# Kernel tuning notes

Measured on AMD Instinct MI355X. Metric: run time of the kernel, lower is better.

The kernel has to match this reference:

```python
import jax, jax.numpy as jnp
import numpy as np

SL, BS, E, H, PF, STRIDE, SHIFT = 2048, 2, 1024, 16, 16, 1, 0
DH = E // H  # 64


def setup_inputs() -> dict:
    key = jax.random.key(0)
    ks = jax.random.split(key, 6)
    s = 0.02
    return {
        'x': jax.random.normal(ks[0], (SL, BS, E), jnp.float32),
        'ln_g': jnp.ones((E,), jnp.float32),
        'ln_b': jnp.zeros((E,), jnp.float32),
        'Wq': jax.random.normal(ks[1], (E, E), jnp.float32) * s,
        'bq': jnp.zeros((E,), jnp.float32),
        'Wk': jax.random.normal(ks[2], (E, E), jnp.float32) * s,
        'bk': jnp.zeros((E,), jnp.float32),
        'Wv': jax.random.normal(ks[3], (E, E), jnp.float32) * s,
        'bv': jnp.zeros((E,), jnp.float32),
        'Wo': jax.random.normal(ks[4], (E, E), jnp.float32) * s,
        'bo': jnp.zeros((E,), jnp.float32),
    }


def _layernorm(x, g, b, eps=1e-5):
    m = x.mean(-1, keepdims=True)
    v = jnp.var(x, axis=-1, keepdims=True)
    return (x - m) * jax.lax.rsqrt(v + eps) * g + b


def _sparsify(context, h):
    # faithful to sparsify(): r = (arange(h)+1)*stride - pf + shift (+ arange(pf)), mod c
    c = context.shape[0]
    base = (jnp.arange(h) + 1) * STRIDE - PF + SHIFT          # [h]
    idx = (base[None, :] + jnp.arange(PF)[:, None]) % c       # [pf, h]
    return context[idx.reshape(-1)].reshape(PF, h, context.shape[1], context.shape[2])


def reference(x, ln_g, ln_b, Wq, bq, Wk, bk, Wv, bv, Wo, bo):
    sl, bs, e = x.shape
    residual = x
    xn = _layernorm(x, ln_g, ln_b)
    # gather pf-sized local context window per query position (modular wrap)
    fetch = _sparsify(xn, sl)                                  # [pf, sl, bs, E]
    # per-token query (length-1) attending to its pf gathered keys
    q = (xn @ Wq + bq).reshape(sl, bs, H, DH)                  # [sl,bs,H,dh]
    k = (fetch @ Wk + bk).reshape(PF, sl, bs, H, DH)           # [pf,sl,bs,H,dh]
    v = (fetch @ Wv + bv).reshape(PF, sl, bs, H, DH)
    scale = 1.0 / jnp.sqrt(jnp.float32(DH))
    scores = jnp.einsum('sbhd,psbhd->sbhp', q, k) * scale      # [sl,bs,H,pf]
    attn = jax.nn.softmax(scores, axis=-1)
    out = jnp.einsum('sbhp,psbhd->sbhd', attn, v).reshape(sl, bs, e)
    out = out @ Wo + bo                                        # output projection
    # dropout is a no-op in eval
    return residual + out
```

## Files before the change

kernel.cpp:

```cpp
#include <hip/hip_runtime.h>
#include <cstdint>
#include <cstddef>

#define SLEN 2048
#define BSZ  2
#define EDIM 1024
#define NHEAD 16
#define DHEAD 64
#define PFW  16
#define NTOK (SLEN*BSZ)

typedef __attribute__((ext_vector_type(8))) short short8;
typedef __attribute__((ext_vector_type(4))) float floatx4;
typedef __attribute__((ext_vector_type(4))) int   int4v;

__device__ __forceinline__ short f2bf(float f) {
  union { float f; uint32_t u; } v; v.f = f;
  uint32_t r = v.u + 0x7fffu + ((v.u >> 16) & 1u);
  return (short)(r >> 16);
}
__device__ __forceinline__ float bf2f(short s) {
  union { uint32_t u; float f; } v; v.u = ((uint32_t)(uint16_t)s) << 16;
  return v.f;
}
__device__ __forceinline__ int q8(float f, float inv) {
  int q = __float2int_rn(f * inv);
  return min(127, max(-127, q));
}

__device__ __forceinline__ void async16(const void* g, void* l) {
  __builtin_amdgcn_global_load_lds((const __attribute__((address_space(1))) void*)g,
                                   (__attribute__((address_space(3))) void*)l,
                                   16, 0, 0);
}

__global__ __launch_bounds__(256) void prep_kernel(
    const float* __restrict__ x, const float* __restrict__ g,
    const float* __restrict__ b, char* __restrict__ xn_i8,
    float* __restrict__ xn_scl,
    const float* __restrict__ W0, const float* __restrict__ W1,
    const float* __restrict__ W2, const float* __restrict__ W3,
    short* __restrict__ Wt_base)
{
  const int bid = blockIdx.x;
  const int tid = threadIdx.x;

  if (bid < NTOK) {
    const int row = bid;
    const float4 v = ((const float4*)(x + (size_t)row * EDIM))[tid];
    float s  = v.x + v.y + v.z + v.w;
    float ss = v.x * v.x + v.y * v.y + v.z * v.z + v.w * v.w;
#pragma unroll
    for (int off = 32; off; off >>= 1) {
      s  += __shfl_xor(s, off);
      ss += __shfl_xor(ss, off);
    }
    __shared__ float ws_s[4], ws_ss[4], ws_m[4];
    const int lane = tid & 63, wave = tid >> 6;
    if (lane == 0) { ws_s[wave] = s; ws_ss[wave] = ss; }
    __syncthreads();
    s  = ws_s[0] + ws_s[1] + ws_s[2] + ws_s[3];
    ss = ws_ss[0] + ws_ss[1] + ws_ss[2] + ws_ss[3];

    const float mean = s * (1.0f / EDIM);
    const float var  = ss * (1.0f / EDIM) - mean * mean;
    const float rs   = rsqrtf(var + 1e-5f);

    const float4 gv = ((const float4*)g)[tid];
    const float4 bv = ((const float4*)b)[tid];
    const float n0 = (v.x - mean) * rs * gv.x + bv.x;
    const float n1 = (v.y - mean) * rs * gv.y + bv.y;
    const float n2 = (v.z - mean) * rs * gv.z + bv.z;
    const float n3 = (v.w - mean) * rs * gv.w + bv.w;

    float am = fmaxf(fmaxf(fabsf(n0), fabsf(n1)), fmaxf(fabsf(n2), fabsf(n3)));
#pragma unroll
    for (int off = 32; off; off >>= 1) am = fmaxf(am, __shfl_xor(am, off));
    if (lane == 0) ws_m[wave] = am;
    __syncthreads();
    am = fmaxf(fmaxf(ws_m[0], ws_m[1]), fmaxf(ws_m[2], ws_m[3]));

    const float inv = (am > 1e-30f) ? 127.0f / am : 0.0f;
    const int q0 = q8(n0, inv), q1 = q8(n1, inv), q2 = q8(n2, inv), q3 = q8(n3, inv);
    const uint32_t pack = (uint32_t)(q0 & 0xff) | ((uint32_t)(q1 & 0xff) << 8) |
                          ((uint32_t)(q2 & 0xff) << 16) | ((uint32_t)(q3 & 0xff) << 24);
    ((uint32_t*)(xn_i8 + (size_t)row * EDIM))[tid] = pack;
    if (tid == 0) xn_scl[row] = am * (1.0f / 127.0f);
  } else {
    const int t = bid - NTOK;
    const int z = t >> 10;
    const int rem = t & 1023;
    const int n0 = (rem & 31) * 32;
    const int k0 = (rem >> 5) * 32;
    const float* W = (z == 0) ? W0 : (z == 1) ? W1 : (z == 2) ? W2 : W3;
    short* Wt = Wt_base + (size_t)z * EDIM * EDIM;

    __shared__ float tile[32][33];
    const int tx = tid & 31;
    const int ty = tid >> 5;
#pragma unroll
    for (int i = 0; i < 4; ++i)
      tile[ty + i * 8][tx] = W[(size_t)(k0 + ty + i * 8) * EDIM + n0 + tx];
    __syncthreads();
#pragma unroll
    for (int i = 0; i < 4; ++i)
      Wt[(size_t)(n0 + ty + i * 8) * EDIM + k0 + tx] = f2bf(tile[tx][ty + i * 8]);
  }
}

__global__ __launch_bounds__(256) void quant_w(
    const short* __restrict__ Wt, char* __restrict__ w_i8,
    float* __restrict__ w_scl)
{
  const int R = blockIdx.x;
  const int tid = threadIdx.x;
  const short4 s4 = ((const short4*)(Wt + (size_t)R * EDIM))[tid];
  const float w0 = bf2f(s4.x), w1 = bf2f(s4.y), w2 = bf2f(s4.z), w3 = bf2f(s4.w);

  float am = fmaxf(fmaxf(fabsf(w0), fabsf(w1)), fmaxf(fabsf(w2), fabsf(w3)));
#pragma unroll
  for (int off = 32; off; off >>= 1) am = fmaxf(am, __shfl_xor(am, off));
  __shared__ float wm[4];
  const int lane = tid & 63, wave = tid >> 6;
  if (lane == 0) wm[wave] = am;
  __syncthreads();
  am = fmaxf(fmaxf(wm[0], wm[1]), fmaxf(wm[2], wm[3]));

  const float inv = (am > 1e-30f) ? 127.0f / am : 0.0f;
  const int q0 = q8(w0, inv), q1 = q8(w1, inv), q2 = q8(w2, inv), q3 = q8(w3, inv);
  const uint32_t pack = (uint32_t)(q0 & 0xff) | ((uint32_t)(q1 & 0xff) << 8) |
                        ((uint32_t)(q2 & 0xff) << 16) | ((uint32_t)(q3 & 0xff) << 24);
  ((uint32_t*)(w_i8 + (size_t)R * EDIM))[tid] = pack;
  if (tid == 0) w_scl[R] = am * (1.0f / 127.0f);
}

__global__ __launch_bounds__(256) void gemm_qkv_i8(
    const char* __restrict__ xn_i8, const float* __restrict__ xn_scl,
    const char* __restrict__ w_i8, const float* __restrict__ w_scl,
    const float* __restrict__ bq, const float* __restrict__ bk,
    const float* __restrict__ bv, short* __restrict__ qkv_base)
{
  __shared__ __align__(16) char As[128 * 64];
  __shared__ __align__(16) char Bs[128 * 64];

  const int bid  = blockIdx.x;
  const int xcd  = bid & 7;
  const int slot = bid >> 3;
  const int nz   = xcd * 3 + slot / 32;
  const int mt   = slot & 31;
  const int z    = nz >> 3;
  const int nt   = nz & 7;

  const char*  Bt   = w_i8 + (size_t)z * EDIM * EDIM;
  const float* bscl = w_scl + z * EDIM;
  const float* bias = (z == 0) ? bq : (z == 1) ? bk : bv;
  short* out        = qkv_base + (size_t)z * NTOK * EDIM;

  const int bm = mt * 128;
  const int bn = nt * 128;
  const int tid  = threadIdx.x;
  const int lane = tid & 63;
  const int wave = tid >> 6;

  int4v acc[4][4];
#pragma unroll
  for (int i = 0; i < 4; ++i)
#pragma unroll
    for (int j = 0; j < 4; ++j) { int4v zz = {0, 0, 0, 0}; acc[i][j] = zz; }

  const int lrow  = lane >> 2;
  const int lcolB = (lane & 3) * 16;
  const char* gA0 = xn_i8 + (size_t)(bm + wave * 32 + lrow) * EDIM + lcolB;
  const char* gA1 = gA0 + (size_t)16 * EDIM;
  const char* gB0 = Bt + (size_t)(bn + wave * 32 + lrow) * EDIM + lcolB;
  const char* gB1 = gB0 + (size_t)16 * EDIM;
  char* lA0 = As + wave * 2048;
  char* lA1 = lA0 + 1024;
  char* lB0 = Bs + wave * 2048;
  char* lB1 = lB0 + 1024;

  const int wm  = (wave >> 1) * 64;
  const int wn  = (wave & 1) * 64;
  const int fr  = lane & 15;
  const int fqB = (lane >> 4) * 16;

  for (int k0 = 0; k0 < EDIM; k0 += 64) {
    async16(gA0, lA0); async16(gA1, lA1);
    async16(gB0, lB0); async16(gB1, lB1);
    gA0 += 64; gA1 += 64; gB0 += 64; gB1 += 64;
    __syncthreads();

    int4v af[4], bf[4];
#pragma unroll
    for (int mi = 0; mi < 4; ++mi)
      af[mi] = *(const int4v*)(As + (size_t)(wm + mi * 16 + fr) * 64 + fqB);
#pragma unroll
    for (int ni = 0; ni < 4; ++ni)
      bf[ni] = *(const int4v*)(Bs + (size_t)(wn + ni * 16 + fr) * 64 + fqB);
#pragma unroll
    for (int mi = 0; mi < 4; ++mi)
#pragma unroll
      for (int ni = 0; ni < 4; ++ni)
        acc[mi][ni] = __builtin_amdgcn_mfma_i32_16x16x64_i8(
            af[mi], bf[ni], acc[mi][ni], 0, 0, 0);
    __syncthreads();
  }

  const int r0 = bm + wm + ((lane >> 4) * 4);
  const int c0 = bn + wn + (lane & 15);
#pragma unroll
  for (int mi = 0; mi < 4; ++mi) {
    float sa[4];
#pragma unroll
    for (int r = 0; r < 4; ++r) sa[r] = xn_scl[r0 + mi * 16 + r];
#pragma unroll
    for (int ni = 0; ni < 4; ++ni) {
      const int4v v = acc[mi][ni];
      const int col = c0 + ni * 16;
      const float sb = bscl[col];
      const float bb = bias[col];
#pragma unroll
      for (int r = 0; r < 4; ++r) {
        const int row = r0 + mi * 16 + r;
        out[(size_t)row * EDIM + col] = f2bf((float)v[r] * (sa[r] * sb) + bb);
      }
    }
  }
}

__global__ __launch_bounds__(256) void gemm_o_i8(
    const char* __restrict__ A8, const float* __restrict__ a_scl,
    const char* __restrict__ w_i8, const float* __restrict__ w_scl,
    const float* __restrict__ bo, const float* __restrict__ residual,
    float* __restrict__ out)
{
  __shared__ __align__(16) char As[64 * 64];
  __shared__ __align__(16) char Bs[128 * 64];
  __shared__ float sa_lds[64 * 17];

  const int bm = blockIdx.x * 64;
  const int bn = blockIdx.y * 128;
  const int tid  = threadIdx.x;
  const int lane = tid & 63;
  const int wave = tid >> 6;

#pragma unroll
  for (int i = 0; i < 4; ++i) {
    const int e = tid + i * 256;
    const int row = e >> 4, h = e & 15;
    sa_lds[row * 17 + h] = a_scl[(size_t)(bm + row) * NHEAD + h];
  }

  floatx4 facc[2][4];
#pragma unroll
  for (int i = 0; i < 2; ++i)
#pragma unroll
    for (int j = 0; j < 4; ++j) { floatx4 zz = {0.f, 0.f, 0.f, 0.f}; facc[i][j] = zz; }

  const int lrow  = lane >> 2;
  const int lcolB = (lane & 3) * 16;
  const char* gA0 = A8 + (size_t)(bm + wave * 16 + lrow) * EDIM + lcolB;
  const char* gB0 = w_i8 + (size_t)3 * EDIM * EDIM +
                    (size_t)(bn + wave * 32 + lrow) * EDIM + lcolB;
  const char* gB1 = gB0 + (size_t)16 * EDIM;
  char* lA0 = As + wave * 1024;
  char* lB0 = Bs + wave * 2048;
  char* lB1 = lB0 + 1024;

  const int wm  = (wave >> 1) * 32;
  const int wn  = (wave & 1) * 64;
  const int fr  = lane & 15;
  const int fqB = (lane >> 4) * 16;
  const int q4  = lane >> 4;

  for (int ki = 0; ki < 16; ++ki) {
    async16(gA0, lA0);
    async16(gB0, lB0); async16(gB1, lB1);
    gA0 += 64; gB0 += 64; gB1 += 64;
    __syncthreads();

    int4v af[2], bf[4];
#pragma unroll
    for (int mi = 0; mi < 2; ++mi)
      af[mi] = *(const int4v*)(As + (size_t)(wm + mi * 16 + fr) * 64 + fqB);
#pragma unroll
    for (int ni = 0; ni < 4; ++ni)
      bf[ni] = *(const int4v*)(Bs + (size_t)(wn + ni * 16 + fr) * 64 + fqB);

    float sa_v[2][4];
#pragma unroll
    for (int mi = 0; mi < 2; ++mi)
#pragma unroll
      for (int r = 0; r < 4; ++r)
        sa_v[mi][r] = sa_lds[(wm + mi * 16 + q4 * 4 + r) * 17 + ki];

#pragma unroll
    for (int mi = 0; mi < 2; ++mi)
#pragma unroll
      for (int ni = 0; ni < 4; ++ni) {
        const int4v zz = {0, 0, 0, 0};
        const int4v t = __builtin_amdgcn_mfma_i32_16x16x64_i8(
            af[mi], bf[ni], zz, 0, 0, 0);
#pragma unroll
        for (int r = 0; r < 4; ++r)
          facc[mi][ni][r] += sa_v[mi][r] * (float)t[r];
      }
    __syncthreads();
  }

  const int r0 = bm + wm + q4 * 4;
  const int c0 = bn + wn + (lane & 15);
#pragma unroll
  for (int mi = 0; mi < 2; ++mi)
#pragma unroll
    for (int ni = 0; ni < 4; ++ni) {
      const int col = c0 + ni * 16;
      const float sb = w_scl[3 * EDIM + col];
      const float bb = bo[col];
#pragma unroll
      for (int r = 0; r < 4; ++r) {
        const int row = r0 + mi * 16 + r;
        const size_t idx = (size_t)row * EDIM + col;
        out[idx] = residual[idx] + facc[mi][ni][r] * sb + bb;
      }
    }
}

#define VT_LD 80
#define PB_LD 40

__global__ __launch_bounds__(256) void attn_mfma(
    const short* __restrict__ Q, const short* __restrict__ K,
    const short* __restrict__ V, char* __restrict__ O8,
    float* __restrict__ a_scl)
{
  const int tid  = threadIdx.x;
  const int lane = tid & 63;
  const int wave = tid >> 6;
  const int quad = lane >> 4;
  const int l16  = lane & 15;

  const int bh = blockIdx.y;
  const int h  = bh & (NHEAD - 1);
  const int b  = bh >> 4;
  const int s_blk = blockIdx.x * 64;
  const int col0  = h * DHEAD;

  __shared__ __align__(16) short VT[64 * VT_LD];
  __shared__ __align__(16) short Pb[4][16 * PB_LD];

  for (int task = tid; task < 320; task += 256) {
    const int kp  = task >> 3;
    const int dg  = task & 7;
    const int kk0 = kp * 2;
    int sA = s_blk - 15 + kk0;
    int sB = sA + 1;
    if (sA < 0) sA += SLEN;  if (sA >= SLEN) sA -= SLEN;
    if (sB < 0) sB += SLEN;  if (sB >= SLEN) sB -= SLEN;
    const short8 vA = *(const short8*)(V + (size_t)(sA * BSZ + b) * EDIM + col0 + dg * 8);
    const short8 vB = *(const short8*)(V + (size_t)(sB * BSZ + b) * EDIM + col0 + dg * 8);
#pragma unroll
    for (int j = 0; j < 8; ++j) {
      const int d = dg * 8 + j;
      const uint32_t pack = (uint32_t)(uint16_t)vA[j] | ((uint32_t)(uint16_t)vB[j] << 16);
      *(uint32_t*)&VT[d * VT_LD + kk0] = pack;
    }
  }

  const int sw = s_blk + wave * 16;
  short8 aq[2];
  {
    const size_t base = (size_t)((sw + l16) * BSZ + b) * EDIM + col0 + quad * 8;
    aq[0] = *(const short8*)(Q + base);
    aq[1] = *(const short8*)(Q + base + 32);
  }
  short8 bkf[2][2];
#pragma unroll
  for (int T = 0; T < 2; ++T) {
    int ks = sw - 15 + T * 16 + l16;
    if (ks < 0) ks += SLEN;
    if (ks >= SLEN) ks -= SLEN;
    const size_t base = (size_t)(ks * BSZ + b) * EDIM + col0 + quad * 8;
    bkf[T][0] = *(const short8*)(K + base);
    bkf[T][1] = *(const short8*)(K + base + 32);
  }

  floatx4 S[2];
  { floatx4 zz = {0.f, 0.f, 0.f, 0.f}; S[0] = zz; S[1] = zz; }
#pragma unroll
  for (int T = 0; T < 2; ++T) {
    S[T] = __builtin_amdgcn_mfma_f32_16x16x32_bf16(aq[0], bkf[T][0], S[T], 0, 0, 0);
    S[T] = __builtin_amdgcn_mfma_f32_16x16x32_bf16(aq[1], bkf[T][1], S[T], 0, 0, 0);
  }

  float sc[2][4];
#pragma unroll
  for (int T = 0; T < 2; ++T)
#pragma unroll
    for (int r = 0; r < 4; ++r) {
      const int m = quad * 4 + r;
      const int c = T * 16 + l16;
      const int d = c - m;
      sc[T][r] = (d >= 0 && d <= 15) ? S[T][r] * 0.125f : -1e30f;
    }
  float mx[4], sm[4];
#pragma unroll
  for (int r = 0; r < 4; ++r) mx[r] = fmaxf(sc[0][r], sc[1][r]);
#pragma unroll
  for (int off = 1; off <= 8; off <<= 1)
#pragma unroll
    for (int r = 0; r < 4; ++r) mx[r] = fmaxf(mx[r], __shfl_xor(mx[r], off));
  float p[2][4];
#pragma unroll
  for (int r = 0; r < 4; ++r) {
    p[0][r] = __expf(sc[0][r] - mx[r]);
    p[1][r] = __expf(sc[1][r] - mx[r]);
    sm[r] = p[0][r] + p[1][r];
  }
#pragma unroll
  for (int off = 1; off <= 8; off <<= 1)
#pragma unroll
    for (int r = 0; r < 4; ++r) sm[r] += __shfl_xor(sm[r], off);

  __syncthreads();

  short* Pw = Pb[wave];
#pragma unroll
  for (int T = 0; T < 2; ++T)
#pragma unroll
    for (int r = 0; r < 4; ++r) {
      const int m = quad * 4 + r;
      const int c = T * 16 + l16;
      Pw[m * PB_LD + c] = f2bf(p[T][r]);
    }
  __syncthreads();
  const short8 ap = *(const short8*)(Pw + l16 * PB_LD + quad * 8);

  floatx4 Oacc[4];
  { floatx4 zz = {0.f, 0.f, 0.f, 0.f}; Oacc[0] = zz; Oacc[1] = zz; Oacc[2] = zz; Oacc[3] = zz; }
#pragma unroll
  for (int nt = 0; nt < 4; ++nt) {
    const short8 bv = *(const short8*)(VT + (nt * 16 + l16) * VT_LD + wave * 16 + quad * 8);
    Oacc[nt] = __builtin_amdgcn_mfma_f32_16x16x32_bf16(ap, bv, Oacc[nt], 0, 0, 0);
  }

  float vv[4][4];
  float am[4] = {0.f, 0.f, 0.f, 0.f};
#pragma unroll
  for (int nt = 0; nt < 4; ++nt)
#pragma unroll
    for (int r = 0; r < 4; ++r) {
      const float v = Oacc[nt][r] / sm[r];
      vv[nt][r] = v;
      am[r] = fmaxf(am[r], fabsf(v));
    }
#pragma unroll
  for (int off = 1; off <= 8; off <<= 1)
#pragma unroll
    for (int r = 0; r < 4; ++r) am[r] = fmaxf(am[r], __shfl_xor(am[r], off));

  float inv[4];
#pragma unroll
  for (int r = 0; r < 4; ++r) inv[r] = (am[r] > 1e-30f) ? 127.0f / am[r] : 0.0f;

#pragma unroll
  for (int nt = 0; nt < 4; ++nt)
#pragma unroll
    for (int r = 0; r < 4; ++r) {
      const int m = quad * 4 + r;
      const int row = (sw + m) * BSZ + b;
      O8[(size_t)row * EDIM + col0 + nt * 16 + l16] = (char)q8(vv[nt][r], inv[r]);
    }
  if (l16 == 0) {
#pragma unroll
    for (int r = 0; r < 4; ++r) {
      const int m = quad * 4 + r;
      const int row = (sw + m) * BSZ + b;
      a_scl[(size_t)row * NHEAD + h] = am[r] * (1.0f / 127.0f);
    }
  }
}

extern "C" void kernel_launch(void* const* d_in, const int* in_sizes, int n_in,
                              void* d_out, int out_size, void* d_ws, size_t ws_size,
                              hipStream_t stream) {
  const float* x    = (const float*)d_in[0];
  const float* ln_g = (const float*)d_in[1];
  const float* ln_b = (const float*)d_in[2];
  const float* Wq   = (const float*)d_in[3];
  const float* bq   = (const float*)d_in[4];
  const float* Wk   = (const float*)d_in[5];
  const float* bk   = (const float*)d_in[6];
  const float* Wv   = (const float*)d_in[7];
  const float* bv   = (const float*)d_in[8];
  const float* Wo   = (const float*)d_in[9];
  const float* bo   = (const float*)d_in[10];
  float* out = (float*)d_out;

  char* ws = (char*)d_ws;
  char*  xn_i8   = ws;
  short* Wt      = (short*)(ws + ((size_t)4  << 20));
  char*  w_i8    = ws + ((size_t)12 << 20);
  short* QKV     = (short*)(ws + ((size_t)16 << 20));
  char*  attn_i8 = ws + ((size_t)40 << 20);
  float* xn_scl  = (float*)(ws + ((size_t)44 << 20));
  float* w_scl   = (float*)(ws + ((size_t)44 << 20) + (1 << 16));
  float* a_scl   = (float*)(ws + ((size_t)44 << 20) + (2 << 16));

  prep_kernel<<<NTOK + 4096, 256, 0, stream>>>(x, ln_g, ln_b, xn_i8, xn_scl,
                                               Wq, Wk, Wv, Wo, Wt);
  quant_w<<<4 * EDIM, 256, 0, stream>>>(Wt, w_i8, w_scl);
  gemm_qkv_i8<<<768, 256, 0, stream>>>(xn_i8, xn_scl, w_i8, w_scl,
                                       bq, bk, bv, QKV);
  attn_mfma<<<dim3(SLEN / 64, BSZ * NHEAD), 256, 0, stream>>>(
      QKV, QKV + (size_t)NTOK * EDIM, QKV + (size_t)2 * NTOK * EDIM,
      attn_i8, a_scl);
  gemm_o_i8<<<dim3(NTOK / 64, EDIM / 128), 256, 0, stream>>>(
      attn_i8, a_scl, w_i8, w_scl, bo, x, out);
}
```

Before: 152.1 us.

## Rewrite QKV int8 GEMM with 256x256 tiles and 4-stage async LDS pipeline

Replaces the 128x128 single-buffer QKV int8 GEMM with a 512-thread, 256x256-tile kernel. It uses a 4-deep ring of LDS buffers filled by async global-to-LDS loads, with three stages kept in flight through explicit vmcnt waits and raw barriers. It also XOR-swizzles the LDS layout to cut bank conflicts and raises wave priority around the MFMA block. The aim is to hide global-load latency and raise data reuse per block. The trade-off is 128KB of LDS, heavier register use and only 192 blocks, which may underfill the CUs.

```diff
diff --git a/kernel.cpp b/kernel.cpp
--- a/kernel.cpp
+++ b/kernel.cpp
@@ -33,6 +33,8 @@
                                    (__attribute__((address_space(3))) void*)l,
                                    16, 0, 0);
 }
+
+#define VMCNT(n) asm volatile("s_waitcnt vmcnt(" #n ")" ::: "memory")
 
 __global__ __launch_bounds__(256) void prep_kernel(
     const float* __restrict__ x, const float* __restrict__ g,
@@ -134,96 +136,113 @@
   if (tid == 0) w_scl[R] = am * (1.0f / 127.0f);
 }
 
-__global__ __launch_bounds__(256) void gemm_qkv_i8(
+__global__ __launch_bounds__(512, 2) void gemm_qkv256(
     const char* __restrict__ xn_i8, const float* __restrict__ xn_scl,
     const char* __restrict__ w_i8, const float* __restrict__ w_scl,
     const float* __restrict__ bq, const float* __restrict__ bk,
     const float* __restrict__ bv, short* __restrict__ qkv_base)
 {
-  __shared__ __align__(16) char As[128 * 64];
-  __shared__ __align__(16) char Bs[128 * 64];
-
-  const int bid  = blockIdx.x;
-  const int xcd  = bid & 7;
-  const int slot = bid >> 3;
-  const int nz   = xcd * 3 + slot / 32;
-  const int mt   = slot & 31;
-  const int z    = nz >> 3;
-  const int nt   = nz & 7;
-
-  const char*  Bt   = w_i8 + (size_t)z * EDIM * EDIM;
-  const float* bscl = w_scl + z * EDIM;
+  __shared__ __align__(16) char lds[4][32768];
+
+  const int bid = blockIdx.x;
+  const int lin = (bid & 7) * 24 + (bid >> 3);
+  const int mt  = lin & 15;
+  const int nt  = lin >> 4;
+  const int z   = nt >> 2;
+  const int bm  = mt * 256;
+  const int bnz = (nt & 3) * 256;
+
   const float* bias = (z == 0) ? bq : (z == 1) ? bk : bv;
-  short* out        = qkv_base + (size_t)z * NTOK * EDIM;
-
-  const int bm = mt * 128;
-  const int bn = nt * 128;
-  const int tid  = threadIdx.x;
-  const int lane = tid & 63;
-  const int wave = tid >> 6;
-
-  int4v acc[4][4];
-#pragma unroll
-  for (int i = 0; i < 4; ++i)
-#pragma unroll
-    for (int j = 0; j < 4; ++j) { int4v zz = {0, 0, 0, 0}; acc[i][j] = zz; }
-
-  const int lrow  = lane >> 2;
-  const int lcolB = (lane & 3) * 16;
-  const char* gA0 = xn_i8 + (size_t)(bm + wave * 32 + lrow) * EDIM + lcolB;
-  const char* gA1 = gA0 + (size_t)16 * EDIM;
-  const char* gB0 = Bt + (size_t)(bn + wave * 32 + lrow) * EDIM + lcolB;
-  const char* gB1 = gB0 + (size_t)16 * EDIM;
-  char* lA0 = As + wave * 2048;
-  char* lA1 = lA0 + 1024;
-  char* lB0 = Bs + wave * 2048;
-  char* lB1 = lB0 + 1024;
-
-  const int wm  = (wave >> 1) * 64;
-  const int wn  = (wave & 1) * 64;
-  const int fr  = lane & 15;
-  const int fqB = (lane >> 4) * 16;
-
-  for (int k0 = 0; k0 < EDIM; k0 += 64) {
-    async16(gA0, lA0); async16(gA1, lA1);
-    async16(gB0, lB0); async16(gB1, lB1);
-    gA0 += 64; gA1 += 64; gB0 += 64; gB1 += 64;
-    __syncthreads();
-
-    int4v af[4], bf[4];
-#pragma unroll
-    for (int mi = 0; mi < 4; ++mi)
-      af[mi] = *(const int4v*)(As + (size_t)(wm + mi * 16 + fr) * 64 + fqB);
+  short* out = qkv_base + (size_t)z * NTOK * EDIM;
+
+  const int tid = threadIdx.x;
+  const int wv  = tid >> 6;
+  const int ln  = tid & 63;
+  const int q   = ln >> 4;
+  const int l16 = ln & 15;
+  const int wm  = wv >> 2;
+  const int wn  = wv & 3;
+
+  const int sr = tid >> 2;
+  const int sc = ((tid & 3) * 16) ^ ((sr & 3) * 16);
+  const char* gA0 = xn_i8 + (size_t)(bm + sr) * EDIM + sc;
+  const char* gA1 = gA0 + (size_t)128 * EDIM;
+  const char* gB0 = w_i8 + ((size_t)z << 20) + (size_t)(bnz + sr) * EDIM + sc;
+  const char* gB1 = gB0 + (size_t)128 * EDIM;
+  const int wbase = wv * 1024;
+
+#define QSTAGE(tt) do { \
+    char* s_ = lds[(tt) & 3]; \
+    async16(gA0 + (tt) * 64, s_ + wbase); \
+    async16(gA1 + (tt) * 64, s_ + 8192 + wbase); \
+    async16(gB0 + (tt) * 64, s_ + 16384 + wbase); \
+    async16(gB1 + (tt) * 64, s_ + 24576 + wbase); \
+  } while (0)
+
+  const int swz  = (q * 16) ^ ((l16 & 3) * 16);
+  const int aoff = (wm * 128 + l16) * 64 + swz;
+  const int boff = 16384 + (wn * 64 + l16) * 64 + swz;
+
+  int4v acc[8][4];
+#pragma unroll
+  for (int mi = 0; mi < 8; ++mi)
+#pragma unroll
+    for (int ni = 0; ni < 4; ++ni) { int4v zz = {0, 0, 0, 0}; acc[mi][ni] = zz; }
+
+  QSTAGE(0); QSTAGE(1); QSTAGE(2);
+  VMCNT(8);
+  __builtin_amdgcn_s_barrier();
+  __builtin_amdgcn_sched_barrier(0);
+
+#pragma unroll
+  for (int t = 0; t < 16; ++t) {
+    if (t + 3 < 16) QSTAGE(t + 3);
+
+    const char* sl = lds[t & 3];
+    int4v bf[4], af[8];
 #pragma unroll
     for (int ni = 0; ni < 4; ++ni)
-      bf[ni] = *(const int4v*)(Bs + (size_t)(wn + ni * 16 + fr) * 64 + fqB);
-#pragma unroll
-    for (int mi = 0; mi < 4; ++mi)
+      bf[ni] = *(const int4v*)(sl + boff + ni * 1024);
+#pragma unroll
+    for (int mi = 0; mi < 8; ++mi)
+      af[mi] = *(const int4v*)(sl + aoff + mi * 1024);
+
+    __builtin_amdgcn_s_setprio(1);
+#pragma unroll
+    for (int mi = 0; mi < 8; ++mi)
 #pragma unroll
       for (int ni = 0; ni < 4; ++ni)
         acc[mi][ni] = __builtin_amdgcn_mfma_i32_16x16x64_i8(
             af[mi], bf[ni], acc[mi][ni], 0, 0, 0);
-    __syncthreads();
-  }
-
-  const int r0 = bm + wm + ((lane >> 4) * 4);
-  const int c0 = bn + wn + (lane & 15);
-#pragma unroll
-  for (int mi = 0; mi < 4; ++mi) {
+    __builtin_amdgcn_s_setprio(0);
+
+    if (t < 15) {
+      if (t <= 12)      VMCNT(8);
+      else if (t == 13) VMCNT(4);
+      else              VMCNT(0);
+      __builtin_amdgcn_s_barrier();
+      __builtin_amdgcn_sched_barrier(0);
+    }
+  }
+#undef QSTAGE
+
+  const int rbase = bm + wm * 128 + q * 4;
+  const int cbl   = bnz + wn * 64 + l16;
+#pragma unroll
+  for (int mi = 0; mi < 8; ++mi) {
     float sa[4];
 #pragma unroll
-    for (int r = 0; r < 4; ++r) sa[r] = xn_scl[r0 + mi * 16 + r];
+    for (int r = 0; r < 4; ++r) sa[r] = xn_scl[rbase + mi * 16 + r];
 #pragma unroll
     for (int ni = 0; ni < 4; ++ni) {
+      const int c  = cbl + ni * 16;
+      const float sb = w_scl[z * EDIM + c];
+      const float bb = bias[c];
       const int4v v = acc[mi][ni];
-      const int col = c0 + ni * 16;
-      const float sb = bscl[col];
-      const float bb = bias[col];
-#pragma unroll
-      for (int r = 0; r < 4; ++r) {
-        const int row = r0 + mi * 16 + r;
-        out[(size_t)row * EDIM + col] = f2bf((float)v[r] * (sa[r] * sb) + bb);
-      }
+#pragma unroll
+      for (int r = 0; r < 4; ++r)
+        out[(size_t)(rbase + mi * 16 + r) * EDIM + c] =
+            f2bf((float)v[r] * (sa[r] * sb) + bb);
     }
   }
 }
@@ -510,7 +529,7 @@
   prep_kernel<<<NTOK + 4096, 256, 0, stream>>>(x, ln_g, ln_b, xn_i8, xn_scl,
                                                Wq, Wk, Wv, Wo, Wt);
   quant_w<<<4 * EDIM, 256, 0, stream>>>(Wt, w_i8, w_scl);
-  gemm_qkv_i8<<<768, 256, 0, stream>>>(xn_i8, xn_scl, w_i8, w_scl,
+  gemm_qkv256<<<192, 512, 0, stream>>>(xn_i8, xn_scl, w_i8, w_scl,
                                        bq, bk, bv, QKV);
   attn_mfma<<<dim3(SLEN / 64, BSZ * NHEAD), 256, 0, stream>>>(
       QKV, QKV + (size_t)NTOK * EDIM, QKV + (size_t)2 * NTOK * EDIM,
```

After: 151.9 us. No clear change (-0.2%).
